# Kernel tuning notes

Measured on AMD Instinct MI355X. Metric: run time of the kernel, lower is better.

Reference implementation:

```python
import jax, jax.numpy as jnp
import numpy as np

N_NODES = 100000
N_EDGES = 1600000
HIDDEN = 64


def gcn_conv(x, edge_index, W, b):
    """PyG GCNConv: add self-loops, symmetric deg^{-1/2} normalization, scatter-add."""
    n = x.shape[0]
    h = x @ W  # [N, F_out]
    loop = jnp.arange(n, dtype=edge_index.dtype)
    src = jnp.concatenate([edge_index[0], loop])  # [E+N]
    dst = jnp.concatenate([edge_index[1], loop])
    deg = jax.ops.segment_sum(jnp.ones_like(dst, dtype=h.dtype), dst, num_segments=n)
    dinv = jnp.where(deg > 0, jax.lax.rsqrt(jnp.maximum(deg, 1e-12)), 0.0)
    norm = dinv[src] * dinv[dst]  # [E+N]
    msg = h[src] * norm[:, None]  # gather + scale
    out = jax.ops.segment_sum(msg, dst, num_segments=n)  # scatter-add
    return out + b


def setup_inputs() -> dict:
    key = jax.random.key(0)
    k = jax.random.split(key, 6)
    x = jax.random.normal(k[0], (N_NODES, HIDDEN), dtype=jnp.float32)
    edge_index = jax.random.randint(k[1], (2, N_EDGES), 0, N_NODES, dtype=jnp.int32)
    s = 1.0 / np.sqrt(HIDDEN)
    W1 = jax.random.normal(k[2], (HIDDEN, HIDDEN), dtype=jnp.float32) * s
    b1 = jnp.zeros((HIDDEN,), dtype=jnp.float32)
    W2 = jax.random.normal(k[3], (HIDDEN, HIDDEN), dtype=jnp.float32) * s
    b2 = jnp.zeros((HIDDEN,), dtype=jnp.float32)
    return {"x": x, "edge_index": edge_index, "W1": W1, "b1": b1, "W2": W2, "b2": b2}


def reference(x, edge_index, W1, b1, W2, b2):
    # Faithful to source: conv1 applied twice, relu, dropout (eval -> identity), conv2, log_softmax.
    h = gcn_conv(x, edge_index, W1, b1)
    h = jax.nn.relu(gcn_conv(h, edge_index, W1, b1))
    # F.dropout(training=self.training): identity in eval mode
    h = gcn_conv(h, edge_index, W2, b2)
    return jax.nn.log_softmax(h, axis=1)
```

## Files before the change

kernel.cpp:

```cpp
#include <hip/hip_runtime.h>
#include <hip/hip_bf16.h>

#define HID 64

typedef float f32x4 __attribute__((ext_vector_type(4)));

__device__ __forceinline__ unsigned short f2bf(float f) {
    unsigned u = __float_as_uint(f);
    return (unsigned short)((u + 0x7fffu + ((u >> 16) & 1u)) >> 16);
}
__device__ __forceinline__ void acc8(float* a, uint4 v) {
    a[0] += __uint_as_float(v.x << 16);
    a[1] += __uint_as_float(v.x & 0xffff0000u);
    a[2] += __uint_as_float(v.y << 16);
    a[3] += __uint_as_float(v.y & 0xffff0000u);
    a[4] += __uint_as_float(v.z << 16);
    a[5] += __uint_as_float(v.z & 0xffff0000u);
    a[6] += __uint_as_float(v.w << 16);
    a[7] += __uint_as_float(v.w & 0xffff0000u);
}


__global__ __launch_bounds__(256) void hist_part_kernel(
    const int* __restrict__ dst, int* __restrict__ cnt, int E, int psz) {
    int part = blockIdx.x & 7, chunk = blockIdx.x >> 3;
    int i = chunk * 256 + threadIdx.x;
    if (i >= E) return;
    int d = __builtin_nontemporal_load(&dst[i]);
    if (d / psz == part) atomicAdd(&cnt[d], 1);
}

__global__ __launch_bounds__(256) void bsum_kernel(const int* __restrict__ cnt,
                                                   int* __restrict__ bsums, int N) {
    __shared__ int s[256];
    int tid = threadIdx.x, i = blockIdx.x * 256 + tid;
    s[tid] = (i < N) ? cnt[i] : 0;
    __syncthreads();
    for (int o = 128; o > 0; o >>= 1) {
        if (tid < o) s[tid] += s[tid + o];
        __syncthreads();
    }
    if (tid == 0) bsums[blockIdx.x] = s[0];
}

__global__ __launch_bounds__(512) void scan_bsums_kernel(int* __restrict__ bsums, int nblk) {
    __shared__ int s[512];
    int tid = threadIdx.x;
    int orig = (tid < nblk) ? bsums[tid] : 0;
    s[tid] = orig;
    __syncthreads();
    for (int off = 1; off < 512; off <<= 1) {
        int v = (tid >= off) ? s[tid - off] : 0;
        __syncthreads();
        s[tid] += v;
        __syncthreads();
    }
    if (tid < nblk) bsums[tid] = s[tid] - orig;
}

__global__ __launch_bounds__(256) void rowptr_kernel(
    const int* __restrict__ cnt, const int* __restrict__ bsums,
    int4* __restrict__ nodeinfo, int* __restrict__ cursor, int N) {
    __shared__ int s[256];
    int tid = threadIdx.x, i = blockIdx.x * 256 + tid;
    int c = (i < N) ? cnt[i] : 0;
    s[tid] = c;
    __syncthreads();
    for (int off = 1; off < 256; off <<= 1) {
        int v = (tid >= off) ? s[tid - off] : 0;
        __syncthreads();
        s[tid] += v;
        __syncthreads();
    }
    if (i < N) {
        int excl = s[tid] - c + bsums[blockIdx.x];
        cursor[i] = excl;
        int4 ni;
        ni.x = excl;
        ni.y = c;
        ni.z = (int)__float_as_uint(rsqrtf((float)c + 1.0f));
        ni.w = 0;
        nodeinfo[i] = ni;
    }
}

__global__ __launch_bounds__(256) void fill_part_kernel(
    const int* __restrict__ src, const int* __restrict__ dst,
    int* __restrict__ cursor, int* __restrict__ col, int E, int psz) {
    int part = blockIdx.x & 7, chunk = blockIdx.x >> 3;
    int i = chunk * 256 + threadIdx.x;
    if (i >= E) return;
    int d = __builtin_nontemporal_load(&dst[i]);
    if (d / psz == part) {
        int s = __builtin_nontemporal_load(&src[i]);
        int p = atomicAdd(&cursor[d], 1);
        __builtin_nontemporal_store(s, &col[p]);
    }
}

__device__ __forceinline__ void gather64(
    const uint4* __restrict__ g4, const int* __restrict__ col,
    int beg, int deg, int n, int N, int lane, float* t) {
    int eighth = lane >> 3, fo = lane & 7;
    float a0[8] = {}, a1[8] = {};
    for (int base = 0; base < deg; base += 64) {
        int rem = deg - base; rem = rem > 64 ? 64 : rem;
        int c = (lane < rem) ? __builtin_nontemporal_load(&col[beg + base + lane]) : N;
        int groups = (rem + 7) >> 3;
        int j = 0;
        for (; j + 2 <= groups; j += 2) {
            int s0 = __shfl(c, 8 * (j + 0) + eighth, 64);
            int s1 = __shfl(c, 8 * (j + 1) + eighth, 64);
            uint4 v0 = g4[(size_t)s0 * 8 + fo];
            uint4 v1 = g4[(size_t)s1 * 8 + fo];
            acc8(a0, v0); acc8(a1, v1);
        }
        if (j < groups) {
            int s0 = __shfl(c, 8 * j + eighth, 64);
            uint4 v0 = g4[(size_t)s0 * 8 + fo];
            acc8(a0, v0);
        }
    }
    float sf[8] = {};
    acc8(sf, g4[(size_t)n * 8 + fo]);
#pragma unroll
    for (int k = 0; k < 8; ++k) {
        float s = a0[k] + a1[k];
        s += __shfl_xor(s, 8, 64);
        s += __shfl_xor(s, 16, 64);
        s += __shfl_xor(s, 32, 64);
        t[k] = s + sf[k];
    }
}


__global__ __launch_bounds__(256) void gemm_scale_kernel(
    const float* __restrict__ X, const float* __restrict__ W,
    const int4* __restrict__ nodeinfo, unsigned short* __restrict__ g, int N) {
    int tid = threadIdx.x, w = tid >> 6, lane = tid & 63;
    float Wreg[64];
#pragma unroll
    for (int k = 0; k < HID; ++k) Wreg[k] = W[k * HID + lane];
    int ngrp = (N + 4) / 4;
    for (int grp = blockIdx.x; grp < ngrp; grp += gridDim.x) {
        int row = grp * 4 + w;
        if (row > N) continue;
        if (row == N) { __builtin_nontemporal_store((unsigned short)0, &g[(size_t)N * HID + lane]); continue; }
        float xv = __builtin_nontemporal_load(&X[(size_t)row * HID + lane]);
        float dn = __uint_as_float(__builtin_amdgcn_readfirstlane((unsigned)nodeinfo[row].z));
        float acc = 0.f;
#pragma unroll
        for (int k = 0; k < HID; ++k) acc = fmaf(__shfl(xv, k, 64), Wreg[k], acc);
        __builtin_nontemporal_store(f2bf(acc * dn), &g[(size_t)row * HID + lane]);
    }
}


template <bool RELU>
__global__ __launch_bounds__(256) void agg_gemm_kernel(
    const unsigned short* __restrict__ g_in, const int4* __restrict__ nodeinfo,
    const int* __restrict__ col, const float* __restrict__ bias,
    const float* __restrict__ W, unsigned short* __restrict__ g_out, int N) {
    int tid = threadIdx.x, w = tid >> 6, lane = tid & 63;
    int fo = lane & 7;
    float Wreg[64];
#pragma unroll
    for (int k = 0; k < HID; ++k) Wreg[k] = W[k * HID + lane];
    float bb[8];
#pragma unroll
    for (int j = 0; j < 8; ++j) bb[j] = bias[8 * fo + j];
    const uint4* g4 = (const uint4*)g_in;
    int ngrp = (N + 4) / 4;
    for (int grp = blockIdx.x; grp < ngrp; grp += gridDim.x) {
        int n = grp * 4 + w;
        if (n > N) continue;
        if (n == N) { __builtin_nontemporal_store((unsigned short)0, &g_out[(size_t)N * HID + lane]); continue; }
        int4 ni = nodeinfo[n];
        int beg  = __builtin_amdgcn_readfirstlane(ni.x);
        int deg  = __builtin_amdgcn_readfirstlane(ni.y);
        float dn = __uint_as_float(__builtin_amdgcn_readfirstlane((unsigned)ni.z));
        float t[8];
        gather64(g4, col, beg, deg, n, N, lane, t);
        float o[8];
#pragma unroll
        for (int j = 0; j < 8; ++j) {
            o[j] = fmaf(dn, t[j], bb[j]);
            if (RELU) o[j] = fmaxf(o[j], 0.f);
        }
        float acc = 0.f;
#pragma unroll
        for (int q = 0; q < 8; ++q)
#pragma unroll
            for (int j = 0; j < 8; ++j)
                acc = fmaf(__shfl(o[j], q, 64), Wreg[8 * q + j], acc);
        __builtin_nontemporal_store(f2bf(acc * dn), &g_out[(size_t)n * HID + lane]);
    }
}


__global__ __launch_bounds__(256) void agg_lsm_kernel(
    const unsigned short* __restrict__ g_in, const int4* __restrict__ nodeinfo,
    const int* __restrict__ col, const float* __restrict__ bias,
    float* __restrict__ out, int N) {
    int tid = threadIdx.x;
    int n = blockIdx.x * 4 + (tid >> 6);
    if (n >= N) return;
    int lane = tid & 63;
    int eighth = lane >> 3, fo = lane & 7;
    int4 ni = nodeinfo[n];
    int beg  = __builtin_amdgcn_readfirstlane(ni.x);
    int deg  = __builtin_amdgcn_readfirstlane(ni.y);
    float dn = __uint_as_float(__builtin_amdgcn_readfirstlane((unsigned)ni.z));
    const uint4* g4 = (const uint4*)g_in;
    float t[8];
    gather64(g4, col, beg, deg, n, N, lane, t);
    float v[8];
#pragma unroll
    for (int k = 0; k < 8; ++k) v[k] = fmaf(dn, t[k], bias[8 * fo + k]);
    float mx = v[0];
#pragma unroll
    for (int k = 1; k < 8; ++k) mx = fmaxf(mx, v[k]);
    mx = fmaxf(mx, __shfl_xor(mx, 1, 64));
    mx = fmaxf(mx, __shfl_xor(mx, 2, 64));
    mx = fmaxf(mx, __shfl_xor(mx, 4, 64));
    float sum = 0.f;
#pragma unroll
    for (int k = 0; k < 8; ++k) sum += expf(v[k] - mx);
    sum += __shfl_xor(sum, 1, 64);
    sum += __shfl_xor(sum, 2, 64);
    sum += __shfl_xor(sum, 4, 64);
    float ls = mx + logf(sum);
    if (eighth == 0) {
        f32x4 o0 = {v[0] - ls, v[1] - ls, v[2] - ls, v[3] - ls};
        f32x4 o1 = {v[4] - ls, v[5] - ls, v[6] - ls, v[7] - ls};
        f32x4* op = (f32x4*)out;
        __builtin_nontemporal_store(o0, &op[(size_t)n * 16 + 2 * fo]);
        __builtin_nontemporal_store(o1, &op[(size_t)n * 16 + 2 * fo + 1]);
    }
}


static inline size_t alignup(size_t x) { return (x + 255) & ~(size_t)255; }

extern "C" void kernel_launch(void* const* d_in, const int* in_sizes, int n_in,
                              void* d_out, int out_size, void* d_ws, size_t ws_size,
                              hipStream_t stream) {
    const float* x  = (const float*)d_in[0];
    const int*   ei = (const int*)d_in[1];
    const float* W1 = (const float*)d_in[2];
    const float* b1 = (const float*)d_in[3];
    const float* W2 = (const float*)d_in[4];
    const float* b2 = (const float*)d_in[5];

    const int N = in_sizes[0] / HID;
    const int E = in_sizes[1] / 2;
    const int* src = ei;
    const int* dst = ei + E;

    const int nblk = (N + 255) / 256;
    const int psz  = (N + 7) / 8;

    char* w = (char*)d_ws;
    unsigned short* gA       = (unsigned short*)w; w += alignup((size_t)(N + 1) * HID * 2);
    unsigned short* gB       = (unsigned short*)w; w += alignup((size_t)(N + 1) * HID * 2);
    int4*           nodeinfo = (int4*)w;           w += alignup((size_t)N * 16);
    int*            cnt      = (int*)w;            w += alignup((size_t)N * 4);
    int*            cursor   = (int*)w;            w += alignup((size_t)N * 4);
    int*            col      = (int*)w;            w += alignup((size_t)E * 4);
    int*            bsums    = (int*)w;            w += alignup((size_t)nblk * 4);

    const int egrid  = (E + 255) / 256;
    const int ngrid  = (N + 3) / 4;
    const int gsgrid = 2048;

    (void)hipMemsetAsync(cnt, 0, (size_t)N * sizeof(int), stream);
    hist_part_kernel<<<egrid * 8, 256, 0, stream>>>(dst, cnt, E, psz);
    bsum_kernel<<<nblk, 256, 0, stream>>>(cnt, bsums, N);
    scan_bsums_kernel<<<1, 512, 0, stream>>>(bsums, nblk);
    rowptr_kernel<<<nblk, 256, 0, stream>>>(cnt, bsums, nodeinfo, cursor, N);
    fill_part_kernel<<<egrid * 8, 256, 0, stream>>>(src, dst, cursor, col, E, psz);

    gemm_scale_kernel<<<gsgrid, 256, 0, stream>>>(x, W1, nodeinfo, gA, N);
    agg_gemm_kernel<false><<<gsgrid, 256, 0, stream>>>(gA, nodeinfo, col, b1, W1, gB, N);
    agg_gemm_kernel<true><<<gsgrid, 256, 0, stream>>>(gB, nodeinfo, col, b1, W2, gA, N);
    agg_lsm_kernel<<<ngrid, 256, 0, stream>>>(gA, nodeinfo, col, b2, (float*)d_out, N);
}
```

Measured before the change: 498.1 us.

## Prefetch next node's row info and column indices; move dense weights into LDS

The aggregation kernels become persistent grid-stride loops that software-pipeline the per-node metadata and the first 64 column indices of the next node while the current node gathers. The per-row 64x64 GEMMs now read weights and activations from shared memory instead of holding W in 64 registers and broadcasting with shuffles, which cuts register pressure and shuffle traffic. Zero padding rows are written with memsets instead of inside the kernels, and the column fill now uses regular stores so col stays in cache. The LDS reads may hit bank conflicts, and the extra prefetched state adds registers.

```diff
diff --git a/kernel.cpp b/kernel.cpp
--- a/kernel.cpp
+++ b/kernel.cpp
@@ -94,18 +94,18 @@
     if (d / psz == part) {
         int s = __builtin_nontemporal_load(&src[i]);
         int p = atomicAdd(&cursor[d], 1);
-        __builtin_nontemporal_store(s, &col[p]);
-    }
-}
-
-__device__ __forceinline__ void gather64(
+        col[p] = s;
+    }
+}
+
+__device__ __forceinline__ void gather64_pre(
     const uint4* __restrict__ g4, const int* __restrict__ col,
-    int beg, int deg, int n, int N, int lane, float* t) {
+    int beg, int deg, int c, int n, int N, int lane, float* t) {
     int eighth = lane >> 3, fo = lane & 7;
     float a0[8] = {}, a1[8] = {};
-    for (int base = 0; base < deg; base += 64) {
-        int rem = deg - base; rem = rem > 64 ? 64 : rem;
-        int c = (lane < rem) ? __builtin_nontemporal_load(&col[beg + base + lane]) : N;
+    int base = 0;
+    while (true) {
+        int rem = deg - base; if (rem > 64) rem = 64;
         int groups = (rem + 7) >> 3;
         int j = 0;
         for (; j + 2 <= groups; j += 2) {
@@ -120,6 +120,10 @@
             uint4 v0 = g4[(size_t)s0 * 8 + fo];
             acc8(a0, v0);
         }
+        base += 64;
+        if (base >= deg) break;
+        int r2 = deg - base;
+        c = (lane < r2) ? __builtin_nontemporal_load(&col[beg + base + lane]) : N;
     }
     float sf[8] = {};
     acc8(sf, g4[(size_t)n * 8 + fo]);
@@ -137,21 +141,23 @@
 __global__ __launch_bounds__(256) void gemm_scale_kernel(
     const float* __restrict__ X, const float* __restrict__ W,
     const int4* __restrict__ nodeinfo, unsigned short* __restrict__ g, int N) {
-    int tid = threadIdx.x, w = tid >> 6, lane = tid & 63;
-    float Wreg[64];
-#pragma unroll
-    for (int k = 0; k < HID; ++k) Wreg[k] = W[k * HID + lane];
-    int ngrp = (N + 4) / 4;
+    __shared__ float Ws[HID * HID];
+    __shared__ float xs[4][HID];
+    int tid = threadIdx.x;
+    for (int i = tid; i < HID * HID; i += 256) Ws[i] = W[i];
+    __syncthreads();
+    int w = tid >> 6, c = tid & 63;
+    float* xsw = xs[w];
+    int ngrp = (N + 3) / 4;
     for (int grp = blockIdx.x; grp < ngrp; grp += gridDim.x) {
         int row = grp * 4 + w;
-        if (row > N) continue;
-        if (row == N) { __builtin_nontemporal_store((unsigned short)0, &g[(size_t)N * HID + lane]); continue; }
-        float xv = __builtin_nontemporal_load(&X[(size_t)row * HID + lane]);
-        float dn = __uint_as_float(__builtin_amdgcn_readfirstlane((unsigned)nodeinfo[row].z));
+        if (row >= N) continue;
+        xsw[c] = __builtin_nontemporal_load(&X[(size_t)row * HID + c]);
+        float dn = __uint_as_float((unsigned)__builtin_amdgcn_readfirstlane(nodeinfo[row].z));
         float acc = 0.f;
 #pragma unroll
-        for (int k = 0; k < HID; ++k) acc = fmaf(__shfl(xv, k, 64), Wreg[k], acc);
-        __builtin_nontemporal_store(f2bf(acc * dn), &g[(size_t)row * HID + lane]);
+        for (int k = 0; k < HID; ++k) acc = fmaf(xsw[k], Ws[k * HID + c], acc);
+        __builtin_nontemporal_store(f2bf(acc * dn), &g[(size_t)row * HID + c]);
     }
 }
 
@@ -161,39 +167,75 @@
     const unsigned short* __restrict__ g_in, const int4* __restrict__ nodeinfo,
     const int* __restrict__ col, const float* __restrict__ bias,
     const float* __restrict__ W, unsigned short* __restrict__ g_out, int N) {
-    int tid = threadIdx.x, w = tid >> 6, lane = tid & 63;
-    int fo = lane & 7;
-    float Wreg[64];
-#pragma unroll
-    for (int k = 0; k < HID; ++k) Wreg[k] = W[k * HID + lane];
+    __shared__ float Ws[HID * HID];
+    __shared__ float4 xs4[4][HID / 4];
+    int tid = threadIdx.x;
+    for (int i = tid; i < HID * HID; i += 256) Ws[i] = W[i];
+    __syncthreads();
+    int w = tid >> 6, lane = tid & 63;
+    int eighth = lane >> 3, fo = lane & 7;
+    const uint4* g4 = (const uint4*)g_in;
+    float* xsw = (float*)xs4[w];
     float bb[8];
 #pragma unroll
     for (int j = 0; j < 8; ++j) bb[j] = bias[8 * fo + j];
-    const uint4* g4 = (const uint4*)g_in;
-    int ngrp = (N + 4) / 4;
-    for (int grp = blockIdx.x; grp < ngrp; grp += gridDim.x) {
-        int n = grp * 4 + w;
-        if (n > N) continue;
-        if (n == N) { __builtin_nontemporal_store((unsigned short)0, &g_out[(size_t)N * HID + lane]); continue; }
-        int4 ni = nodeinfo[n];
-        int beg  = __builtin_amdgcn_readfirstlane(ni.x);
-        int deg  = __builtin_amdgcn_readfirstlane(ni.y);
-        float dn = __uint_as_float(__builtin_amdgcn_readfirstlane((unsigned)ni.z));
-        float t[8];
-        gather64(g4, col, beg, deg, n, N, lane, t);
-        float o[8];
-#pragma unroll
-        for (int j = 0; j < 8; ++j) {
-            o[j] = fmaf(dn, t[j], bb[j]);
-            if (RELU) o[j] = fmaxf(o[j], 0.f);
+    const int gdim = gridDim.x;
+    const int ngrp = (N + 3) / 4;
+    int grp = blockIdx.x;
+    if (grp >= ngrp) return;
+
+    int n_cur = grp * 4 + w;
+    bool v_cur = n_cur < N;
+    int4 ni;
+    ni.x = ni.y = ni.z = ni.w = 0;
+    if (v_cur) ni = nodeinfo[n_cur];
+    int beg_cur = __builtin_amdgcn_readfirstlane(ni.x);
+    int deg_cur = __builtin_amdgcn_readfirstlane(ni.y);
+    unsigned dnu_cur = (unsigned)__builtin_amdgcn_readfirstlane(ni.z);
+    int c_cur = (v_cur && lane < deg_cur) ? __builtin_nontemporal_load(&col[beg_cur + lane]) : N;
+
+    int grp_nxt = grp + gdim;
+    int n_nxt = grp_nxt * 4 + w;
+    bool v_nxt = (grp_nxt < ngrp) && (n_nxt < N);
+    int4 ni_nxt;
+    ni_nxt.x = ni_nxt.y = ni_nxt.z = ni_nxt.w = 0;
+    if (v_nxt) ni_nxt = nodeinfo[n_nxt];
+
+    while (true) {
+        int beg_nxt = __builtin_amdgcn_readfirstlane(ni_nxt.x);
+        int deg_nxt = __builtin_amdgcn_readfirstlane(ni_nxt.y);
+        unsigned dnu_nxt = (unsigned)__builtin_amdgcn_readfirstlane(ni_nxt.z);
+        int c_nxt = (v_nxt && lane < deg_nxt) ? __builtin_nontemporal_load(&col[beg_nxt + lane]) : N;
+        int grp_n2 = grp_nxt + gdim;
+        int n_n2 = grp_n2 * 4 + w;
+        bool v_n2 = (grp_n2 < ngrp) && (n_n2 < N);
+        int4 ni_n2;
+        ni_n2.x = ni_n2.y = ni_n2.z = ni_n2.w = 0;
+        if (v_n2) ni_n2 = nodeinfo[n_n2];
+
+        if (v_cur) {
+            float dn = __uint_as_float(dnu_cur);
+            float t[8];
+            gather64_pre(g4, col, beg_cur, deg_cur, c_cur, n_cur, N, lane, t);
+            float o[8];
+#pragma unroll
+            for (int j = 0; j < 8; ++j) {
+                o[j] = fmaf(dn, t[j], bb[j]);
+                if (RELU) o[j] = fmaxf(o[j], 0.f);
+            }
+            if (eighth == 0) {
+                xs4[w][2 * fo]     = make_float4(o[0], o[1], o[2], o[3]);
+                xs4[w][2 * fo + 1] = make_float4(o[4], o[5], o[6], o[7]);
+            }
+            float acc = 0.f;
+#pragma unroll
+            for (int k = 0; k < HID; ++k) acc = fmaf(xsw[k], Ws[k * HID + lane], acc);
+            __builtin_nontemporal_store(f2bf(acc * dn), &g_out[(size_t)n_cur * HID + lane]);
         }
-        float acc = 0.f;
-#pragma unroll
-        for (int q = 0; q < 8; ++q)
-#pragma unroll
-            for (int j = 0; j < 8; ++j)
-                acc = fmaf(__shfl(o[j], q, 64), Wreg[8 * q + j], acc);
-        __builtin_nontemporal_store(f2bf(acc * dn), &g_out[(size_t)n * HID + lane]);
+        if (grp_nxt >= ngrp) break;
+        n_cur = n_nxt; v_cur = v_nxt;
+        beg_cur = beg_nxt; deg_cur = deg_nxt; dnu_cur = dnu_nxt; c_cur = c_nxt;
+        grp_nxt = grp_n2; n_nxt = n_n2; v_nxt = v_n2; ni_nxt = ni_n2;
     }
 }
 
@@ -202,40 +244,78 @@
     const unsigned short* __restrict__ g_in, const int4* __restrict__ nodeinfo,
     const int* __restrict__ col, const float* __restrict__ bias,
     float* __restrict__ out, int N) {
-    int tid = threadIdx.x;
-    int n = blockIdx.x * 4 + (tid >> 6);
-    if (n >= N) return;
-    int lane = tid & 63;
+    int tid = threadIdx.x, w = tid >> 6, lane = tid & 63;
     int eighth = lane >> 3, fo = lane & 7;
-    int4 ni = nodeinfo[n];
-    int beg  = __builtin_amdgcn_readfirstlane(ni.x);
-    int deg  = __builtin_amdgcn_readfirstlane(ni.y);
-    float dn = __uint_as_float(__builtin_amdgcn_readfirstlane((unsigned)ni.z));
     const uint4* g4 = (const uint4*)g_in;
-    float t[8];
-    gather64(g4, col, beg, deg, n, N, lane, t);
-    float v[8];
-#pragma unroll
-    for (int k = 0; k < 8; ++k) v[k] = fmaf(dn, t[k], bias[8 * fo + k]);
-    float mx = v[0];
-#pragma unroll
-    for (int k = 1; k < 8; ++k) mx = fmaxf(mx, v[k]);
-    mx = fmaxf(mx, __shfl_xor(mx, 1, 64));
-    mx = fmaxf(mx, __shfl_xor(mx, 2, 64));
-    mx = fmaxf(mx, __shfl_xor(mx, 4, 64));
-    float sum = 0.f;
-#pragma unroll
-    for (int k = 0; k < 8; ++k) sum += expf(v[k] - mx);
-    sum += __shfl_xor(sum, 1, 64);
-    sum += __shfl_xor(sum, 2, 64);
-    sum += __shfl_xor(sum, 4, 64);
-    float ls = mx + logf(sum);
-    if (eighth == 0) {
-        f32x4 o0 = {v[0] - ls, v[1] - ls, v[2] - ls, v[3] - ls};
-        f32x4 o1 = {v[4] - ls, v[5] - ls, v[6] - ls, v[7] - ls};
-        f32x4* op = (f32x4*)out;
-        __builtin_nontemporal_store(o0, &op[(size_t)n * 16 + 2 * fo]);
-        __builtin_nontemporal_store(o1, &op[(size_t)n * 16 + 2 * fo + 1]);
+    float bb[8];
+#pragma unroll
+    for (int j = 0; j < 8; ++j) bb[j] = bias[8 * fo + j];
+    const int gdim = gridDim.x;
+    const int ngrp = (N + 3) / 4;
+    int grp = blockIdx.x;
+    if (grp >= ngrp) return;
+
+    int n_cur = grp * 4 + w;
+    bool v_cur = n_cur < N;
+    int4 ni;
+    ni.x = ni.y = ni.z = ni.w = 0;
+    if (v_cur) ni = nodeinfo[n_cur];
+    int beg_cur = __builtin_amdgcn_readfirstlane(ni.x);
+    int deg_cur = __builtin_amdgcn_readfirstlane(ni.y);
+    unsigned dnu_cur = (unsigned)__builtin_amdgcn_readfirstlane(ni.z);
+    int c_cur = (v_cur && lane < deg_cur) ? __builtin_nontemporal_load(&col[beg_cur + lane]) : N;
+
+    int grp_nxt = grp + gdim;
+    int n_nxt = grp_nxt * 4 + w;
+    bool v_nxt = (grp_nxt < ngrp) && (n_nxt < N);
+    int4 ni_nxt;
+    ni_nxt.x = ni_nxt.y = ni_nxt.z = ni_nxt.w = 0;
+    if (v_nxt) ni_nxt = nodeinfo[n_nxt];
+
+    while (true) {
+        int beg_nxt = __builtin_amdgcn_readfirstlane(ni_nxt.x);
+        int deg_nxt = __builtin_amdgcn_readfirstlane(ni_nxt.y);
+        unsigned dnu_nxt = (unsigned)__builtin_amdgcn_readfirstlane(ni_nxt.z);
+        int c_nxt = (v_nxt && lane < deg_nxt) ? __builtin_nontemporal_load(&col[beg_nxt + lane]) : N;
+        int grp_n2 = grp_nxt + gdim;
+        int n_n2 = grp_n2 * 4 + w;
+        bool v_n2 = (grp_n2 < ngrp) && (n_n2 < N);
+        int4 ni_n2;
+        ni_n2.x = ni_n2.y = ni_n2.z = ni_n2.w = 0;
+        if (v_n2) ni_n2 = nodeinfo[n_n2];
+
+        if (v_cur) {
+            float dn = __uint_as_float(dnu_cur);
+            float t[8];
+            gather64_pre(g4, col, beg_cur, deg_cur, c_cur, n_cur, N, lane, t);
+            float v[8];
+#pragma unroll
+            for (int k = 0; k < 8; ++k) v[k] = fmaf(dn, t[k], bb[k]);
+            float mx = v[0];
+#pragma unroll
+            for (int k = 1; k < 8; ++k) mx = fmaxf(mx, v[k]);
+            mx = fmaxf(mx, __shfl_xor(mx, 1, 64));
+            mx = fmaxf(mx, __shfl_xor(mx, 2, 64));
+            mx = fmaxf(mx, __shfl_xor(mx, 4, 64));
+            float sum = 0.f;
+#pragma unroll
+            for (int k = 0; k < 8; ++k) sum += expf(v[k] - mx);
+            sum += __shfl_xor(sum, 1, 64);
+            sum += __shfl_xor(sum, 2, 64);
+            sum += __shfl_xor(sum, 4, 64);
+            float ls = mx + logf(sum);
+            if (eighth == 0) {
+                f32x4 o0 = {v[0] - ls, v[1] - ls, v[2] - ls, v[3] - ls};
+                f32x4 o1 = {v[4] - ls, v[5] - ls, v[6] - ls, v[7] - ls};
+                f32x4* op = (f32x4*)out;
+                __builtin_nontemporal_store(o0, &op[(size_t)n_cur * 16 + 2 * fo]);
+                __builtin_nontemporal_store(o1, &op[(size_t)n_cur * 16 + 2 * fo + 1]);
+            }
+        }
+        if (grp_nxt >= ngrp) break;
+        n_cur = n_nxt; v_cur = v_nxt;
+        beg_cur = beg_nxt; deg_cur = deg_nxt; dnu_cur = dnu_nxt; c_cur = c_nxt;
+        grp_nxt = grp_n2; n_nxt = n_n2; v_nxt = v_n2; ni_nxt = ni_n2;
     }
 }
 
@@ -270,8 +350,10 @@
     int*            bsums    = (int*)w;            w += alignup((size_t)nblk * 4);
 
     const int egrid  = (E + 255) / 256;
-    const int ngrid  = (N + 3) / 4;
     const int gsgrid = 2048;
+
+    (void)hipMemsetAsync(gA + (size_t)N * HID, 0, HID * sizeof(unsigned short), stream);
+    (void)hipMemsetAsync(gB + (size_t)N * HID, 0, HID * sizeof(unsigned short), stream);
 
     (void)hipMemsetAsync(cnt, 0, (size_t)N * sizeof(int), stream);
     hist_part_kernel<<<egrid * 8, 256, 0, stream>>>(dst, cnt, E, psz);
@@ -283,5 +365,5 @@
     gemm_scale_kernel<<<gsgrid, 256, 0, stream>>>(x, W1, nodeinfo, gA, N);
     agg_gemm_kernel<false><<<gsgrid, 256, 0, stream>>>(gA, nodeinfo, col, b1, W1, gB, N);
     agg_gemm_kernel<true><<<gsgrid, 256, 0, stream>>>(gB, nodeinfo, col, b1, W2, gA, N);
-    agg_lsm_kernel<<<ngrid, 256, 0, stream>>>(gA, nodeinfo, col, b2, (float*)d_out, N);
-}
+    agg_lsm_kernel<<<gsgrid, 256, 0, stream>>>(gA, nodeinfo, col, b2, (float*)d_out, N);
+}
```

New measurement: 424.8 us. 14.7% less time.
